# Optimization experiments

Measured on AMD Instinct MI355X. Metric: run time of the kernel, lower is better.

## Reference

```python
import jax, jax.numpy as jnp
import numpy as np

E, NH, NL, NP = 256, 8, 4, 4
D = E // NH
SPATIAL_SHAPES = np.array([[100, 134], [50, 67], [25, 34], [13, 17]], dtype=np.int64)
B = 2


def setup_inputs() -> dict:
    key = jax.random.key(0)
    ks = jax.random.split(key, 12)
    Lin = int((SPATIAL_SHAPES[:, 0] * SPATIAL_SHAPES[:, 1]).sum())
    Lq = Lin
    s = 0.02
    return {
        'query': jax.random.normal(ks[0], (Lq, B, E), jnp.float32),
        'value': jax.random.normal(ks[1], (Lin, B, E), jnp.float32),
        'reference_points': jax.random.uniform(ks[2], (B, Lq, NL, 2), jnp.float32),
        'spatial_shapes': SPATIAL_SHAPES,
        'W_value': jax.random.normal(ks[3], (E, E), jnp.float32) * s,
        'b_value': jnp.zeros((E,), jnp.float32),
        'W_offset': jax.random.normal(ks[4], (E, NH * NL * NP * 2), jnp.float32) * s,
        'b_offset': jax.random.normal(ks[5], (NH * NL * NP * 2,), jnp.float32) * 0.5,
        'W_attn': jax.random.normal(ks[6], (E, NH * NL * NP), jnp.float32) * s,
        'b_attn': jnp.zeros((NH * NL * NP,), jnp.float32),
        'W_out': jax.random.normal(ks[7], (E, E), jnp.float32) * s,
        'b_out': jnp.zeros((E,), jnp.float32),
    }


def _ms_deform_attn(value, spatial_shapes, sampling_locations, attention_weights):
    # value: (B, Lin, NH, D); sampling_locations: (B, Lq, NH, NL, NP, 2) in [0,1]
    # attention_weights: (B, Lq, NH, NL, NP)
    b, _, nh, d = value.shape
    lq = sampling_locations.shape[1]
    npnt = sampling_locations.shape[4]
    shapes = np.asarray(spatial_shapes)
    out = jnp.zeros((b, nh, lq, d), value.dtype)
    start = 0
    for l in range(shapes.shape[0]):
        H, W = int(shapes[l, 0]), int(shapes[l, 1])
        vl = value[:, start:start + H * W].transpose(0, 2, 1, 3)  # (B, NH, H*W, D)
        loc = sampling_locations[:, :, :, l].transpose(0, 2, 1, 3, 4)  # (B, NH, Lq, P, 2)
        # grid_sample align_corners=False convention (matches CUDA kernel)
        x = loc[..., 0] * W - 0.5
        y = loc[..., 1] * H - 0.5
        x0 = jnp.floor(x)
        y0 = jnp.floor(y)
        dx = x - x0
        dy = y - y0
        x0i = x0.astype(jnp.int32)
        y0i = y0.astype(jnp.int32)
        acc = jnp.zeros((b, nh, lq, npnt, d), value.dtype)
        corners = [
            (x0i, y0i, (1.0 - dx) * (1.0 - dy)),
            (x0i + 1, y0i, dx * (1.0 - dy)),
            (x0i, y0i + 1, (1.0 - dx) * dy),
            (x0i + 1, y0i + 1, dx * dy),
        ]
        for xi, yi, w in corners:
            valid = ((xi >= 0) & (xi < W) & (yi >= 0) & (yi < H)).astype(value.dtype)
            idx = jnp.clip(yi, 0, W - 1 if False else H - 1) * 0  # placeholder removed below
            idx = jnp.clip(yi, 0, H - 1) * W + jnp.clip(xi, 0, W - 1)  # (B, NH, Lq, P)
            g = jnp.take_along_axis(vl, idx.reshape(b, nh, -1)[..., None], axis=2)
            g = g.reshape(b, nh, lq, npnt, d)
            acc = acc + g * (w * valid)[..., None]
        awl = attention_weights[:, :, :, l].transpose(0, 2, 1, 3)  # (B, NH, Lq, P)
        out = out + jnp.einsum('bhqpd,bhqp->bhqd', acc, awl)
        start += H * W
    return out.transpose(0, 2, 1, 3).reshape(b, lq, nh * d)  # (B, Lq, E)


def reference(query, value, reference_points, spatial_shapes,
              W_value, b_value, W_offset, b_offset, W_attn, b_attn, W_out, b_out):
    q = query.transpose(1, 0, 2)   # (B, Lq, E)
    v = value.transpose(1, 0, 2)   # (B, Lin, E)
    b, lq, _ = q.shape
    lin = v.shape[1]
    v = (v @ W_value + b_value).reshape(b, lin, NH, D)
    offsets = (q @ W_offset + b_offset).reshape(b, lq, NH, NL, NP, 2)
    attn = (q @ W_attn + b_attn).reshape(b, lq, NH, NL, NP)
    attn = jax.nn.softmax(attn, axis=-1)  # softmax over points (as in source)
    shapes_f = jnp.asarray(np.asarray(spatial_shapes), jnp.float32)
    offset_normalizer = jnp.stack([shapes_f[:, 1], shapes_f[:, 0]], -1)  # (NL, 2) = (w, h)
    loc = reference_points[:, :, None, :, None, :] + offsets / offset_normalizer[None, None, None, :, None, :]
    out = _ms_deform_attn(v, spatial_shapes, loc, attn)  # (B, Lq, E)
    out = out @ W_out + b_out
    return out.transpose(1, 0, 2)  # (Lq, B, E)
```

## Files before the change

### kernel.cpp

```cpp
#include <hip/hip_runtime.h>
#include <math.h>

#define LQ    17821
#define MROWS 35642
#define KD    256

typedef __attribute__((ext_vector_type(8))) short bf16x8;
typedef __attribute__((ext_vector_type(4))) float f32x4;
typedef unsigned int u32;

__device__ __forceinline__ short f2bf(float f) {
  union { float f; unsigned u; } c; c.f = f;
  unsigned u = c.u;
  return (short)((u + 0x7fffu + ((u >> 16) & 1u)) >> 16);
}
__device__ __forceinline__ float bf2f(short s) {
  union { unsigned u; float f; } c;
  c.u = ((unsigned)(unsigned short)s) << 16;
  return c.f;
}

__device__ __forceinline__ void gld_lds16(const short* g, short* l) {
  __builtin_amdgcn_global_load_lds(
      (const __attribute__((address_space(1))) u32*)g,
      (__attribute__((address_space(3))) u32*)l, 16, 0, 0);
}

__global__ __launch_bounds__(256) void cvt_pair(
    const float* __restrict__ q, const float* __restrict__ v,
    short* __restrict__ qb, short* __restrict__ vb)
{
  const float* s = blockIdx.y ? v : q;
  short* d = blockIdx.y ? vb : qb;
  int i = (blockIdx.x * 256 + threadIdx.x) * 4;
  if (i < MROWS * KD) {
    float4 x = *(const float4*)(s + i);
    short4 o;
    o.x = f2bf(x.x); o.y = f2bf(x.y); o.z = f2bf(x.z); o.w = f2bf(x.w);
    *(short4*)(d + i) = o;
  }
}

__global__ __launch_bounds__(256) void wtrans_all(
    const float* __restrict__ Wv, const float* __restrict__ Woff,
    const float* __restrict__ Wat, const float* __restrict__ Wout,
    const float* __restrict__ boff, const float* __restrict__ bat,
    short* __restrict__ wT, float* __restrict__ fbias)
{
  int sel = blockIdx.y;
  int idx = blockIdx.x * 256 + threadIdx.x;
  if (sel == 4) {
    if (idx < 384) fbias[idx] = (idx < 256) ? boff[idx] : bat[idx - 256];
    return;
  }
  const float* W = sel == 0 ? Wv : sel == 1 ? Woff : sel == 2 ? Wat : Wout;
  short* Wt = wT + (sel == 0 ? 0 : sel == 1 ? 65536 : sel == 2 ? 131072 : 163840);
  int N = (sel == 2) ? 128 : 256;
  if (idx < N * 256) {
    int n = idx >> 8, k = idx & 255;
    Wt[idx] = f2bf(W[k * N + n]);
  }
}

__global__ __launch_bounds__(256, 3) void gemm_asy(
    const short* __restrict__ A0, const short* __restrict__ A1,
    const short* __restrict__ Bt0, const short* __restrict__ Bt1,
    const float* __restrict__ bias0, const float* __restrict__ bias1,
    short* __restrict__ out0, float* __restrict__ out1,
    int N1, int gybase)
{
  __shared__ short As[128 * 32];
  __shared__ short Bs[128 * 32];

  const int tid = threadIdx.x;
  const int gy = blockIdx.y + gybase;
  const bool sel0 = gy < 2;
  const short* A = sel0 ? A0 : A1;
  const short* Bt = sel0 ? Bt0 : Bt1;
  const float* bias = sel0 ? bias0 : bias1;
  const int bn = (sel0 ? gy : gy - 2) * 128;
  const int bm = blockIdx.x * 128;

  const int wv = tid >> 6;
  const int lane = tid & 63;

  const int srow = lane >> 2;
  const int skel = (lane & 3) * 8;
  const int rA0 = min(bm + wv * 32 + srow, MROWS - 1);
  const int rA1 = min(bm + wv * 32 + 16 + srow, MROWS - 1);
  const short* gA0 = A + (size_t)rA0 * KD + skel;
  const short* gA1 = A + (size_t)rA1 * KD + skel;
  const short* gB0 = Bt + (size_t)(bn + wv * 32 + srow) * KD + skel;
  const short* gB1 = Bt + (size_t)(bn + wv * 32 + 16 + srow) * KD + skel;
  short* lA0 = &As[(wv * 32) * 32];
  short* lA1 = &As[(wv * 32 + 16) * 32];
  short* lB0 = &Bs[(wv * 32) * 32];
  short* lB1 = &Bs[(wv * 32 + 16) * 32];

  const int wm = (wv & 1) * 64;
  const int wn = (wv >> 1) * 64;
  const int ln = lane & 15;
  const int lq = lane >> 4;

  f32x4 acc[4][4];
#pragma unroll
  for (int i = 0; i < 4; ++i)
#pragma unroll
    for (int j = 0; j < 4; ++j) acc[i][j] = (f32x4){0.f, 0.f, 0.f, 0.f};

  for (int k0 = 0; k0 < KD; k0 += 32) {
    __syncthreads();
    gld_lds16(gA0 + k0, lA0);
    gld_lds16(gA1 + k0, lA1);
    gld_lds16(gB0 + k0, lB0);
    gld_lds16(gB1 + k0, lB1);
    __syncthreads();

    bf16x8 af[4], bfm[4];
#pragma unroll
    for (int i = 0; i < 4; ++i)
      af[i] = *(const bf16x8*)&As[(wm + i * 16 + ln) * 32 + lq * 8];
#pragma unroll
    for (int j = 0; j < 4; ++j)
      bfm[j] = *(const bf16x8*)&Bs[(wn + j * 16 + ln) * 32 + lq * 8];
#pragma unroll
    for (int i = 0; i < 4; ++i)
#pragma unroll
      for (int j = 0; j < 4; ++j)
        acc[i][j] = __builtin_amdgcn_mfma_f32_16x16x32_bf16(af[i], bfm[j], acc[i][j], 0, 0, 0);
  }

  const int N = sel0 ? 256 : N1;
#pragma unroll
  for (int j = 0; j < 4; ++j) {
    const int col = bn + wn + j * 16 + ln;
    const float bb = bias[col];
#pragma unroll
    for (int i = 0; i < 4; ++i) {
      const int row0 = bm + wm + i * 16 + lq * 4;
#pragma unroll
      for (int r = 0; r < 4; ++r) {
        const int row = row0 + r;
        if (row < MROWS) {
          float v = acc[i][j][r] + bb;
          if (sel0)
            out0[(size_t)row * 256 + col] = f2bf(v);
          else
            out1[(size_t)row * N + col] = v;
        }
      }
    }
  }
}

__global__ __launch_bounds__(256) void msda_sample(
    const short* __restrict__ vproj, const float* __restrict__ oa,
    const float* __restrict__ refp, short* __restrict__ out)
{
  static constexpr int LVL_H[4] = {100, 50, 25, 13};
  static constexpr int LVL_W[4] = {134, 67, 34, 17};
  static constexpr int LVL_S[4] = {0, 13400, 16750, 17600};

  __shared__ int4   s_off[8 * 8 * 17];
  __shared__ float4 s_w[8 * 8 * 17];

  const int tid = threadIdx.x;
  const int m0 = blockIdx.x * 8;

#pragma unroll
  for (int it = 0; it < 4; ++it) {
    int w = tid + it * 256;
    int mr = w >> 7;
    int rest = w & 127;
    int h = rest >> 4;
    int lp = rest & 15;
    int l = lp >> 2;
    int p = lp & 3;
    int m = m0 + mr;
    if (m < MROWS) {
      int b = m & 1, q = m >> 1;
      const int Hl = LVL_H[l], Wl = LVL_W[l], Sl = LVL_S[l];
      const float fW = (float)Wl, fH = (float)Hl;

      float4 av = *(const float4*)(oa + (size_t)m * 384 + 256 + h * 16 + l * 4);
      float a0 = av.x, a1 = av.y, a2 = av.z, a3 = av.w;
      float mx = fmaxf(fmaxf(a0, a1), fmaxf(a2, a3));
      a0 = __expf(a0 - mx); a1 = __expf(a1 - mx);
      a2 = __expf(a2 - mx); a3 = __expf(a3 - mx);
      float sel = (p == 0) ? a0 : (p == 1) ? a1 : (p == 2) ? a2 : a3;
      float aw = sel / (a0 + a1 + a2 + a3);

      const float* oPtr = oa + (size_t)m * 384 + h * 32 + l * 8 + p * 2;
      float ox = oPtr[0], oy = oPtr[1];
      const float* rPtr = refp + ((size_t)b * LQ + q) * 8 + l * 2;
      float rx = rPtr[0], ry = rPtr[1];

      float x = (rx + ox / fW) * fW - 0.5f;
      float y = (ry + oy / fH) * fH - 0.5f;
      float x0f = floorf(x), y0f = floorf(y);
      float dx = x - x0f, dy = y - y0f;
      int x0 = (int)x0f, y0 = (int)y0f;
      int x1 = x0 + 1, y1 = y0 + 1;

      float w00 = (1.f - dx) * (1.f - dy) * aw;
      float w10 = dx * (1.f - dy) * aw;
      float w01 = (1.f - dx) * dy * aw;
      float w11 = dx * dy * aw;

      bool vx0 = (x0 >= 0) & (x0 < Wl);
      bool vx1 = (x1 >= 0) & (x1 < Wl);
      bool vy0 = (y0 >= 0) & (y0 < Hl);
      bool vy1 = (y1 >= 0) & (y1 < Hl);
      int cx0 = min(max(x0, 0), Wl - 1);
      int cx1 = min(max(x1, 0), Wl - 1);
      int cy0 = min(max(y0, 0), Hl - 1);
      int cy1 = min(max(y1, 0), Hl - 1);

      int r0 = Sl + cy0 * Wl;
      int r1 = Sl + cy1 * Wl;
      int e = (mr * 8 + h) * 17 + lp;
      s_off[e] = make_int4(((r0 + cx0) * 2 + b) << 8,
                           ((r0 + cx1) * 2 + b) << 8,
                           ((r1 + cx0) * 2 + b) << 8,
                           ((r1 + cx1) * 2 + b) << 8);
      s_w[e] = make_float4((vy0 & vx0) ? w00 : 0.f,
                           (vy0 & vx1) ? w10 : 0.f,
                           (vy1 & vx0) ? w01 : 0.f,
                           (vy1 & vx1) ? w11 : 0.f);
    }
  }
  __syncthreads();

  const int mr = tid >> 5;
  const int t = tid & 31;
  const int h = t >> 2;
  const int dq = t & 3;
  const int m = m0 + mr;
  if (m >= MROWS) return;

  const int laneOff = h * 32 + dq * 8;
  const int ebase = (mr * 8 + h) * 17;
  float acc[8];
#pragma unroll
  for (int e = 0; e < 8; ++e) acc[e] = 0.f;

#pragma unroll 4
  for (int lp = 0; lp < 16; ++lp) {
    int4 off = s_off[ebase + lp];
    float4 wv = s_w[ebase + lp];
    bf16x8 u00 = *(const bf16x8*)(vproj + off.x + laneOff);
    bf16x8 u10 = *(const bf16x8*)(vproj + off.y + laneOff);
    bf16x8 u01 = *(const bf16x8*)(vproj + off.z + laneOff);
    bf16x8 u11 = *(const bf16x8*)(vproj + off.w + laneOff);
#pragma unroll
    for (int e = 0; e < 8; ++e) {
      acc[e] = fmaf(wv.x, bf2f(u00[e]), acc[e]);
      acc[e] = fmaf(wv.y, bf2f(u10[e]), acc[e]);
      acc[e] = fmaf(wv.z, bf2f(u01[e]), acc[e]);
      acc[e] = fmaf(wv.w, bf2f(u11[e]), acc[e]);
    }
  }

  bf16x8 o;
#pragma unroll
  for (int e = 0; e < 8; ++e) o[e] = f2bf(acc[e]);
  *(bf16x8*)(out + (size_t)m * 256 + laneOff) = o;
}

extern "C" void kernel_launch(void* const* d_in, const int* in_sizes, int n_in,
                              void* d_out, int out_size, void* d_ws, size_t ws_size,
                              hipStream_t stream)
{
  const float* query = (const float*)d_in[0];
  const float* value = (const float*)d_in[1];
  const float* refp  = (const float*)d_in[2];
  const float* Wv   = (const float*)d_in[4];
  const float* bv   = (const float*)d_in[5];
  const float* Woff = (const float*)d_in[6];
  const float* boff = (const float*)d_in[7];
  const float* Wat  = (const float*)d_in[8];
  const float* bat  = (const float*)d_in[9];
  const float* Wout = (const float*)d_in[10];
  const float* bout = (const float*)d_in[11];
  float* out = (float*)d_out;

  const size_t NELT = (size_t)MROWS * 256;
  short* wT    = (short*)d_ws;
  float* fbias = (float*)(wT + 229376);
  short* qb    = (short*)(fbias + 384);
  short* vb    = qb + NELT;
  short* vproj = vb + NELT;
  float* oa    = (float*)(vproj + NELT);
  short* accb  = vb;

  dim3 blk(256, 1, 1);
  int gm = (MROWS + 127) / 128;

  cvt_pair<<<dim3(8911, 2), blk, 0, stream>>>(query, value, qb, vb);
  wtrans_all<<<dim3(256, 5), blk, 0, stream>>>(Wv, Woff, Wat, Wout, boff, bat, wT, fbias);

  gemm_asy<<<dim3(gm, 5), blk, 0, stream>>>(
      vb, qb, wT, wT + 65536, bv, fbias, vproj, oa, 384, 0);

  msda_sample<<<dim3((MROWS + 7) / 8), blk, 0, stream>>>(vproj, oa, refp, accb);

  gemm_asy<<<dim3(gm, 2), blk, 0, stream>>>(
      accb, accb, wT + 163840, wT + 163840, bout, bout, nullptr, out, 256, 2);
}
```

Measured before the change: 296.2 us.

## Double-buffer GEMM LDS loads, store offsets/attn in bf16, merge prep kernels

The GEMM now double-buffers its LDS tiles, using explicit waitcnt and barriers so the global-to-LDS loads for step t+2 overlap the MFMAs of step t, and occupancy is raised to 4 blocks. The offset/attention projection output is written as bf16 instead of fp32, which halves the traffic the sampling kernel reads. The conversion and weight-transpose kernels are merged into one launch. Bf16 offsets lose precision in the sampling locations, and the hand-coded waitcnt values must match the number of loads in flight.

After: 286.4 us. 1.03x faster.

```diff
diff --git a/kernel.cpp b/kernel.cpp
--- a/kernel.cpp
+++ b/kernel.cpp
@@ -26,51 +26,58 @@
       (__attribute__((address_space(3))) u32*)l, 16, 0, 0);
 }
 
-__global__ __launch_bounds__(256) void cvt_pair(
-    const float* __restrict__ q, const float* __restrict__ v,
-    short* __restrict__ qb, short* __restrict__ vb)
-{
-  const float* s = blockIdx.y ? v : q;
-  short* d = blockIdx.y ? vb : qb;
-  int i = (blockIdx.x * 256 + threadIdx.x) * 4;
-  if (i < MROWS * KD) {
-    float4 x = *(const float4*)(s + i);
-    short4 o;
-    o.x = f2bf(x.x); o.y = f2bf(x.y); o.z = f2bf(x.z); o.w = f2bf(x.w);
-    *(short4*)(d + i) = o;
-  }
-}
-
-__global__ __launch_bounds__(256) void wtrans_all(
+#define WAIT_VM4   { __builtin_amdgcn_s_waitcnt(0x0F74); asm volatile("" ::: "memory"); }
+#define WAIT_VM0   { __builtin_amdgcn_s_waitcnt(0x0F70); asm volatile("" ::: "memory"); }
+#define WAIT_LGKM0 { __builtin_amdgcn_s_waitcnt(0xC07F); asm volatile("" ::: "memory"); }
+#define BARRIER    { asm volatile("" ::: "memory"); __builtin_amdgcn_s_barrier(); asm volatile("" ::: "memory"); }
+
+__global__ __launch_bounds__(256) void prep(
+    const float* __restrict__ query, const float* __restrict__ value,
     const float* __restrict__ Wv, const float* __restrict__ Woff,
     const float* __restrict__ Wat, const float* __restrict__ Wout,
     const float* __restrict__ boff, const float* __restrict__ bat,
+    short* __restrict__ qb, short* __restrict__ vb,
     short* __restrict__ wT, float* __restrict__ fbias)
 {
-  int sel = blockIdx.y;
+  const int y = blockIdx.y;
+  if (y < 2) {
+    const float* s = y ? value : query;
+    short* d = y ? vb : qb;
+    int i = (blockIdx.x * 256 + threadIdx.x) * 4;
+    if (i < MROWS * KD) {
+      float4 x = *(const float4*)(s + i);
+      short4 o;
+      o.x = f2bf(x.x); o.y = f2bf(x.y); o.z = f2bf(x.z); o.w = f2bf(x.w);
+      *(short4*)(d + i) = o;
+    }
+    return;
+  }
   int idx = blockIdx.x * 256 + threadIdx.x;
-  if (sel == 4) {
-    if (idx < 384) fbias[idx] = (idx < 256) ? boff[idx] : bat[idx - 256];
-    return;
-  }
-  const float* W = sel == 0 ? Wv : sel == 1 ? Woff : sel == 2 ? Wat : Wout;
-  short* Wt = wT + (sel == 0 ? 0 : sel == 1 ? 65536 : sel == 2 ? 131072 : 163840);
-  int N = (sel == 2) ? 128 : 256;
-  if (idx < N * 256) {
-    int n = idx >> 8, k = idx & 255;
-    Wt[idx] = f2bf(W[k * N + n]);
-  }
-}
-
-__global__ __launch_bounds__(256, 3) void gemm_asy(
+  if (idx < 229376) {
+    const float* W; int base, N;
+    if (idx < 65536)       { W = Wv;   base = 0;      N = 256; }
+    else if (idx < 131072) { W = Woff; base = 65536;  N = 256; }
+    else if (idx < 163840) { W = Wat;  base = 131072; N = 128; }
+    else                   { W = Wout; base = 163840; N = 256; }
+    int local = idx - base;
+    int n = local >> 8, k = local & 255;
+    wT[idx] = f2bf(W[k * N + n]);
+  } else if (idx < 229376 + 384) {
+    int j = idx - 229376;
+    fbias[j] = (j < 256) ? boff[j] : bat[j - 256];
+  }
+}
+
+template<bool O1BF>
+__global__ __launch_bounds__(256, 4) void gemm_pipe(
     const short* __restrict__ A0, const short* __restrict__ A1,
     const short* __restrict__ Bt0, const short* __restrict__ Bt1,
     const float* __restrict__ bias0, const float* __restrict__ bias1,
-    short* __restrict__ out0, float* __restrict__ out1,
+    short* __restrict__ out0, void* __restrict__ out1v,
     int N1, int gybase)
 {
-  __shared__ short As[128 * 32];
-  __shared__ short Bs[128 * 32];
+  __shared__ short As[2 * 128 * 32];
+  __shared__ short Bs[2 * 128 * 32];
 
   const int tid = threadIdx.x;
   const int gy = blockIdx.y + gybase;
@@ -97,6 +104,14 @@
   short* lB0 = &Bs[(wv * 32) * 32];
   short* lB1 = &Bs[(wv * 32 + 16) * 32];
 
+#define ISSUE(t, buf)                          \
+  {                                            \
+    gld_lds16(gA0 + (t) * 32, lA0 + (buf) * 4096); \
+    gld_lds16(gA1 + (t) * 32, lA1 + (buf) * 4096); \
+    gld_lds16(gB0 + (t) * 32, lB0 + (buf) * 4096); \
+    gld_lds16(gB1 + (t) * 32, lB1 + (buf) * 4096); \
+  }
+
   const int wm = (wv & 1) * 64;
   const int wn = (wv >> 1) * 64;
   const int ln = lane & 15;
@@ -108,27 +123,34 @@
 #pragma unroll
     for (int j = 0; j < 4; ++j) acc[i][j] = (f32x4){0.f, 0.f, 0.f, 0.f};
 
-  for (int k0 = 0; k0 < KD; k0 += 32) {
-    __syncthreads();
-    gld_lds16(gA0 + k0, lA0);
-    gld_lds16(gA1 + k0, lA1);
-    gld_lds16(gB0 + k0, lB0);
-    gld_lds16(gB1 + k0, lB1);
-    __syncthreads();
+  ISSUE(0, 0);
+  ISSUE(1, 1);
+
+#pragma unroll
+  for (int t = 0; t < 8; ++t) {
+    const int buf = t & 1;
+    if (t < 7) { WAIT_VM4; } else { WAIT_VM0; }
+    BARRIER;
 
     bf16x8 af[4], bfm[4];
 #pragma unroll
     for (int i = 0; i < 4; ++i)
-      af[i] = *(const bf16x8*)&As[(wm + i * 16 + ln) * 32 + lq * 8];
+      af[i] = *(const bf16x8*)&As[buf * 4096 + (wm + i * 16 + ln) * 32 + lq * 8];
 #pragma unroll
     for (int j = 0; j < 4; ++j)
-      bfm[j] = *(const bf16x8*)&Bs[(wn + j * 16 + ln) * 32 + lq * 8];
+      bfm[j] = *(const bf16x8*)&Bs[buf * 4096 + (wn + j * 16 + ln) * 32 + lq * 8];
+
+    WAIT_LGKM0;
+    BARRIER;
+    if (t + 2 < 8) ISSUE(t + 2, buf);
+
 #pragma unroll
     for (int i = 0; i < 4; ++i)
 #pragma unroll
       for (int j = 0; j < 4; ++j)
         acc[i][j] = __builtin_amdgcn_mfma_f32_16x16x32_bf16(af[i], bfm[j], acc[i][j], 0, 0, 0);
   }
+#undef ISSUE
 
   const int N = sel0 ? 256 : N1;
 #pragma unroll
@@ -145,8 +167,10 @@
           float v = acc[i][j][r] + bb;
           if (sel0)
             out0[(size_t)row * 256 + col] = f2bf(v);
+          else if (O1BF)
+            ((short*)out1v)[(size_t)row * N + col] = f2bf(v);
           else
-            out1[(size_t)row * N + col] = v;
+            ((float*)out1v)[(size_t)row * N + col] = v;
         }
       }
     }
@@ -154,7 +178,7 @@
 }
 
 __global__ __launch_bounds__(256) void msda_sample(
-    const short* __restrict__ vproj, const float* __restrict__ oa,
+    const short* __restrict__ vproj, const short* __restrict__ oa,
     const float* __restrict__ refp, short* __restrict__ out)
 {
   static constexpr int LVL_H[4] = {100, 50, 25, 13};
@@ -182,16 +206,16 @@
       const int Hl = LVL_H[l], Wl = LVL_W[l], Sl = LVL_S[l];
       const float fW = (float)Wl, fH = (float)Hl;
 
-      float4 av = *(const float4*)(oa + (size_t)m * 384 + 256 + h * 16 + l * 4);
-      float a0 = av.x, a1 = av.y, a2 = av.z, a3 = av.w;
+      short4 a4 = *(const short4*)(oa + (size_t)m * 384 + 256 + h * 16 + l * 4);
+      float a0 = bf2f(a4.x), a1 = bf2f(a4.y), a2 = bf2f(a4.z), a3 = bf2f(a4.w);
       float mx = fmaxf(fmaxf(a0, a1), fmaxf(a2, a3));
       a0 = __expf(a0 - mx); a1 = __expf(a1 - mx);
       a2 = __expf(a2 - mx); a3 = __expf(a3 - mx);
       float sel = (p == 0) ? a0 : (p == 1) ? a1 : (p == 2) ? a2 : a3;
       float aw = sel / (a0 + a1 + a2 + a3);
 
-      const float* oPtr = oa + (size_t)m * 384 + h * 32 + l * 8 + p * 2;
-      float ox = oPtr[0], oy = oPtr[1];
+      const short* oPtr = oa + (size_t)m * 384 + h * 32 + l * 8 + p * 2;
+      float ox = bf2f(oPtr[0]), oy = bf2f(oPtr[1]);
       const float* rPtr = refp + ((size_t)b * LQ + q) * 8 + l * 2;
       float rx = rPtr[0], ry = rPtr[1];
 
@@ -290,20 +314,20 @@
   short* qb    = (short*)(fbias + 384);
   short* vb    = qb + NELT;
   short* vproj = vb + NELT;
-  float* oa    = (float*)(vproj + NELT);
+  short* oa    = vproj + NELT;
   short* accb  = vb;
 
   dim3 blk(256, 1, 1);
   int gm = (MROWS + 127) / 128;
 
-  cvt_pair<<<dim3(8911, 2), blk, 0, stream>>>(query, value, qb, vb);
-  wtrans_all<<<dim3(256, 5), blk, 0, stream>>>(Wv, Woff, Wat, Wout, boff, bat, wT, fbias);
-
-  gemm_asy<<<dim3(gm, 5), blk, 0, stream>>>(
+  prep<<<dim3(8911, 3), blk, 0, stream>>>(
+      query, value, Wv, Woff, Wat, Wout, boff, bat, qb, vb, wT, fbias);
+
+  gemm_pipe<true><<<dim3(gm, 5), blk, 0, stream>>>(
       vb, qb, wT, wT + 65536, bv, fbias, vproj, oa, 384, 0);
 
   msda_sample<<<dim3((MROWS + 7) / 8), blk, 0, stream>>>(vproj, oa, refp, accb);
 
-  gemm_asy<<<dim3(gm, 2), blk, 0, stream>>>(
+  gemm_pipe<false><<<dim3(gm, 2), blk, 0, stream>>>(
       accb, accb, wT + 163840, wT + 163840, bout, bout, nullptr, out, 256, 2);
 }
```
